# Performance work log

Measured on AMD Instinct MI355X. Metric: run time of the kernel, lower is better.

The kernel has to match this reference:

```python
import jax, jax.numpy as jnp
import numpy as np

DIM = 256
HEADS = 8
WS = 8
N = WS * WS
HID = 1024
EPS = 1e-5


def _rel_pos_index():
    ch, cw = np.meshgrid(np.arange(WS), np.arange(WS), indexing='ij')
    coords = np.stack([ch.ravel(), cw.ravel()])  # [2, N]
    rel = coords[:, :, None] - coords[:, None, :]  # [2, N, N]
    rel = rel.transpose(1, 2, 0).astype(np.int64)
    rel[:, :, 0] += WS - 1
    rel[:, :, 1] += WS - 1
    rel[:, :, 0] *= 2 * WS - 1
    return jnp.asarray(rel.sum(-1))  # [N, N]

REL_IDX = _rel_pos_index()


def layer_norm(x, g, b):
    mu = jnp.mean(x, axis=-1, keepdims=True)
    var = jnp.mean(jnp.square(x - mu), axis=-1, keepdims=True)
    return (x - mu) * jax.lax.rsqrt(var + EPS) * g + b


def setup_inputs() -> dict:
    key = jax.random.key(0)
    ks = jax.random.split(key, 12)
    s = 0.02
    return {
        'x': jax.random.normal(ks[0], (32, 4096, DIM), jnp.float32),
        'attn_mask': jnp.zeros((64, N, N), jnp.float32),  # unused (forward sets mask=None)
        'g1': jnp.ones((DIM,), jnp.float32),
        'b1': jnp.zeros((DIM,), jnp.float32),
        'w_qkv': jax.random.normal(ks[1], (3 * DIM, DIM), jnp.float32) * s,
        'b_qkv': jnp.zeros((3 * DIM,), jnp.float32),
        'bias_table': jax.random.normal(ks[2], ((2 * WS - 1) ** 2, HEADS), jnp.float32) * s,
        'w_proj': jax.random.normal(ks[3], (DIM, DIM), jnp.float32) * s,
        'b_proj': jnp.zeros((DIM,), jnp.float32),
        'g2': jnp.ones((DIM,), jnp.float32),
        'b2': jnp.zeros((DIM,), jnp.float32),
        'w_fc1': jax.random.normal(ks[4], (HID, DIM), jnp.float32) * s,
        'b_fc1': jnp.zeros((HID,), jnp.float32),
        'w_fc2': jax.random.normal(ks[5], (DIM, HID), jnp.float32) * s,
        'b_fc2': jnp.zeros((DIM,), jnp.float32),
    }


def reference(x, attn_mask, g1, b1, w_qkv, b_qkv, bias_table, w_proj, b_proj,
              g2, b2, w_fc1, b_fc1, w_fc2, b_fc2):
    B, L, C = x.shape
    H = W = int(np.sqrt(L))
    hd = C // HEADS
    scale = hd ** -0.5

    shortcut = x
    xn = layer_norm(x, g1, b1).reshape(B, H, W, C)
    xw = xn.reshape(B, H // WS, WS, W // WS, WS, C)
    xw = xw.transpose(0, 1, 3, 2, 4, 5).reshape(-1, N, C)  # [B_, N, C]

    qkv = (xw @ w_qkv.T + b_qkv).reshape(-1, N, 3, HEADS, hd)
    q, k, v = [qkv[:, :, i].transpose(0, 2, 1, 3) for i in range(3)]  # [B_, h, N, d]
    attn = jnp.einsum('bhnd,bhmd->bhnm', q * scale, k)
    bias = bias_table[REL_IDX]  # [N, N, h]
    attn = attn + bias.transpose(2, 0, 1)[None]
    attn = jax.nn.softmax(attn, axis=-1)
    out = jnp.einsum('bhnm,bhmd->bhnd', attn, v)
    out = out.transpose(0, 2, 1, 3).reshape(-1, N, C)
    out = out @ w_proj.T + b_proj

    # window reverse
    out = out.reshape(B, H // WS, W // WS, WS, WS, C)
    out = out.transpose(0, 1, 3, 2, 4, 5).reshape(B, L, C)

    x1 = shortcut + out
    h = layer_norm(x1, g2, b2) @ w_fc1.T + b_fc1
    h = jax.nn.gelu(h, approximate=False)
    return x1 + (h @ w_fc2.T + b_fc2)
```

## Files before the change

### kernel.cpp

```cpp
#include <hip/hip_runtime.h>
#include <hip/hip_bf16.h>
#include <hip/hip_fp16.h>

typedef _Float16 f16;
typedef __attribute__((ext_vector_type(8))) _Float16 f16x8;
typedef __attribute__((ext_vector_type(4))) _Float16 f16x4;
typedef __attribute__((ext_vector_type(2))) _Float16 f16x2;
typedef __attribute__((ext_vector_type(4))) float f32x4;

#define AS1(p) ((const __attribute__((address_space(1))) void*)(p))
#define AS3(p) ((__attribute__((address_space(3))) void*)(p))

__global__ __launch_bounds__(256) void cvt_weights(
    const float* __restrict__ wq, const float* __restrict__ wp,
    const float* __restrict__ wf1, const float* __restrict__ wf2,
    f16* __restrict__ o) {
  int i = blockIdx.x * 256 + threadIdx.x;
  float v;
  if (i < 196608)       v = wq[i];
  else if (i < 262144)  v = wp[i - 196608];
  else if (i < 524288)  v = wf1[i - 262144];
  else                  v = wf2[i - 524288];
  o[i] = (f16)v;
}

__global__ __launch_bounds__(256) void prep_bias(
    const float* __restrict__ bt, float* __restrict__ T) {
  const int flat = blockIdx.x * 256 + threadIdx.x;
  const int h = flat >> 12, l = (flat >> 6) & 63, s = flat & 63;
  const int i = s >> 4, j = (s >> 2) & 3, r = s & 3;
  const int n = 16 * i + 4 * (l >> 4) + r;
  const int m = 16 * j + (l & 15);
  const int idx = ((n >> 3) - (m >> 3) + 7) * 15 + ((n & 7) - (m & 7) + 7);
  T[flat] = bt[idx * 8 + h] * 1.4426950408889634f;
}

template<bool PART, typename TIN>
__global__ __launch_bounds__(256) void ln_rows(
    const TIN* __restrict__ x, const float* __restrict__ g,
    const float* __restrict__ b, f16* __restrict__ out) {
  const int t = blockIdx.x * 4 + (threadIdx.x >> 6);
  const int lane = threadIdx.x & 63;
  float v0, v1, v2, v3;
  if constexpr (sizeof(TIN) == 4) {
    const float4 v = ((const float4*)(x + (long)t * 256))[lane];
    v0 = v.x; v1 = v.y; v2 = v.z; v3 = v.w;
  } else {
    const f16x4 v = ((const f16x4*)(x + (long)t * 256))[lane];
    v0 = (float)v[0]; v1 = (float)v[1]; v2 = (float)v[2]; v3 = (float)v[3];
  }
  float s  = v0 + v1 + v2 + v3;
  float ss = v0*v0 + v1*v1 + v2*v2 + v3*v3;
  #pragma unroll
  for (int off = 32; off; off >>= 1) {
    s  += __shfl_xor(s, off);
    ss += __shfl_xor(ss, off);
  }
  const float mu = s * (1.0f / 256.0f);
  const float var = ss * (1.0f / 256.0f) - mu * mu;
  const float rs = rsqrtf(var + 1e-5f);
  const float4 gv = ((const float4*)g)[lane];
  const float4 bv = ((const float4*)b)[lane];
  long row;
  if (PART) {
    const int bI = t >> 12, l = t & 4095;
    const int hh = l >> 6, w2 = l & 63;
    const int wi = bI * 64 + (hh >> 3) * 8 + (w2 >> 3);
    const int n  = (hh & 7) * 8 + (w2 & 7);
    row = (long)wi * 64 + n;
  } else {
    row = t;
  }
  f16x4 o4;
  o4[0] = (f16)((v0 - mu) * rs * gv.x + bv.x);
  o4[1] = (f16)((v1 - mu) * rs * gv.y + bv.y);
  o4[2] = (f16)((v2 - mu) * rs * gv.z + bv.z);
  o4[3] = (f16)((v3 - mu) * rs * gv.w + bv.w);
  *(f16x4*)(out + row * 256 + lane * 4) = o4;
}

template<int EPI, int K>
__global__ __launch_bounds__(256) void gemm_bt(
    const f16* __restrict__ A, const f16* __restrict__ Bw,
    const float* __restrict__ bias, const float* __restrict__ residf,
    const f16* __restrict__ residh,
    f16* __restrict__ outh, float* __restrict__ outf, int N) {
  __shared__ f16 As[128 * 32];
  __shared__ f16 Bs[128 * 32];
  const int tid  = threadIdx.x;
  const int wid  = tid >> 6;
  const int lane = tid & 63;
  const int qd   = lane >> 4;
  const int l16  = lane & 15;
  const int gx  = gridDim.x;
  const int nwg = gx * gridDim.y;
  const int g   = blockIdx.y * gx + blockIdx.x;
  const int gs  = (g & 7) * (nwg >> 3) + (g >> 3);
  const long tM = (long)(gs / gx) * 128;
  const int  tN = (gs % gx) * 128;
  const int srow = lane >> 2;
  const int scol = (lane & 3) * 8;
  const int wm = (wid >> 1) * 64;
  const int wn = (wid & 1) * 64;

  f32x4 acc[4][4];
  #pragma unroll
  for (int i = 0; i < 4; ++i)
    #pragma unroll
    for (int j = 0; j < 4; ++j) acc[i][j] = (f32x4){0.f, 0.f, 0.f, 0.f};

  for (int k0 = 0; k0 < K; k0 += 32) {
    #pragma unroll
    for (int t = 0; t < 2; ++t) {
      const int gidx = wid * 2 + t;
      const int row  = gidx * 16 + srow;
      __builtin_amdgcn_global_load_lds(AS1(A + (tM + row) * K + k0 + scol),
                                       AS3(&As[gidx * 512]), 16, 0, 0);
      __builtin_amdgcn_global_load_lds(AS1(Bw + (long)(tN + row) * K + k0 + scol),
                                       AS3(&Bs[gidx * 512]), 16, 0, 0);
    }
    __syncthreads();
    f16x8 af[4], bf[4];
    #pragma unroll
    for (int i = 0; i < 4; ++i) af[i] = *(const f16x8*)&As[(wm + i * 16 + l16) * 32 + qd * 8];
    #pragma unroll
    for (int j = 0; j < 4; ++j) bf[j] = *(const f16x8*)&Bs[(wn + j * 16 + l16) * 32 + qd * 8];
    #pragma unroll
    for (int i = 0; i < 4; ++i)
      #pragma unroll
      for (int j = 0; j < 4; ++j)
        acc[i][j] = __builtin_amdgcn_mfma_f32_16x16x32_f16(af[i], bf[j], acc[i][j], 0, 0, 0);
    __syncthreads();
  }

  float bb[4];
  #pragma unroll
  for (int j = 0; j < 4; ++j) bb[j] = bias[tN + wn + j * 16 + l16];

  if (EPI == 3) {
    #pragma unroll
    for (int j = 0; j < 4; ++j) {
      const int col = tN + wn + j * 16 + l16;
      #pragma unroll
      for (int i = 0; i < 4; ++i) {
        #pragma unroll
        for (int r = 0; r < 4; ++r) {
          const long row = tM + wm + i * 16 + qd * 4 + r;
          const long off = row * 256 + col;
          outf[off] = (float)residh[off] + acc[i][j][r] + bb[j];
        }
      }
    }
  } else {
    f16* slice = As + wid * 1024;
    const int rrow = lane >> 3;
    const int seg  = lane & 7;
    #pragma unroll
    for (int i = 0; i < 4; ++i) {
      #pragma unroll
      for (int j = 0; j < 4; ++j) {
        #pragma unroll
        for (int r = 0; r < 4; ++r) {
          float v = acc[i][j][r] + bb[j];
          if (EPI == 2) v = 0.5f * v * (1.0f + erff(v * 0.70710678118654752f));
          const int r16 = qd * 4 + r;
          slice[r16 * 64 + ((j * 16 + l16) ^ ((r16 & 7) << 3))] = (f16)v;
        }
      }
      __syncthreads();
      #pragma unroll
      for (int hrow = 0; hrow < 16; hrow += 8) {
        const int lrow = hrow + rrow;
        const f16x8 v8 = *(const f16x8*)(slice + lrow * 64 + (seg ^ (lrow & 7)) * 8);
        const long grow = tM + wm + i * 16 + lrow;
        const int  gc   = tN + wn + seg * 8;
        if (EPI == 1) {
          const int rw = (int)grow;
          const int wi = rw >> 6, n = rw & 63;
          const int bI = wi >> 6, wloc = wi & 63;
          const int hh = (wloc >> 3) * 8 + (n >> 3);
          const int w2 = (wloc & 7) * 8 + (n & 7);
          const long prow = (long)bI * 4096 + hh * 64 + w2;
          const float* rp = residf + prow * 256 + gc;
          f16x8 o;
          #pragma unroll
          for (int k = 0; k < 8; ++k) o[k] = (f16)(rp[k] + (float)v8[k]);
          *(f16x8*)(outh + prow * 256 + gc) = o;
        } else {
          *(f16x8*)(outh + grow * N + gc) = v8;
        }
      }
      __syncthreads();
    }
  }
}

__global__ __launch_bounds__(256, 3) void attn_win(
    const f16* __restrict__ qkv, const float* __restrict__ bt,
    f16* __restrict__ out) {
  __shared__ __align__(16) char SMEM[4 * 12800];
  const int wid = threadIdx.x >> 6, lane = threadIdx.x & 63;
  const int qd = lane >> 4, l16 = lane & 15;
  const int unit = blockIdx.x * 4 + wid;
  const int wi = unit >> 3, h = unit & 7;
  char* W = SMEM + wid * 12800;
  f16* VT = (f16*)W;
  char* Pb = W + 4608;

  const f16* qbase = qkv + (long)wi * 64 * 768 + h * 32;

  f16x8 qa[4], kb[4];
  #pragma unroll
  for (int i = 0; i < 4; ++i)
    qa[i] = *(const f16x8*)(qbase + (16 * i + l16) * 768 + qd * 8);
  #pragma unroll
  for (int j = 0; j < 4; ++j)
    kb[j] = *(const f16x8*)(qbase + 256 + (16 * j + l16) * 768 + qd * 8);

  #pragma unroll
  for (int it = 0; it < 4; ++it) {
    const f16x8 v8 = *(const f16x8*)(qbase + 512 + (16 * it + l16) * 768 + qd * 8);
    #pragma unroll
    for (int e = 0; e < 8; ++e)
      VT[(qd * 8 + e) * 72 + 16 * it + l16] = v8[e];
  }

  f32x4 S[4][4];
  #pragma unroll
  for (int i = 0; i < 4; ++i)
    #pragma unroll
    for (int j = 0; j < 4; ++j) S[i][j] = (f32x4){0.f, 0.f, 0.f, 0.f};
  #pragma unroll
  for (int i = 0; i < 4; ++i)
    #pragma unroll
    for (int j = 0; j < 4; ++j)
      S[i][j] = __builtin_amdgcn_mfma_f32_16x16x32_f16(qa[i], kb[j], S[i][j], 0, 0, 0);

  const float SC = 0.17677669529663687f * 1.4426950408889634f;
  const float* Tb = bt + ((h * 64 + lane) << 6);
  #pragma unroll
  for (int i = 0; i < 4; ++i) {
    f32x4 b0 = *(const f32x4*)(Tb + i * 16);
    f32x4 b1 = *(const f32x4*)(Tb + i * 16 + 4);
    f32x4 b2 = *(const f32x4*)(Tb + i * 16 + 8);
    f32x4 b3 = *(const f32x4*)(Tb + i * 16 + 12);
    #pragma unroll
    for (int r = 0; r < 4; ++r) {
      S[i][0][r] = S[i][0][r] * SC + b0[r];
      S[i][1][r] = S[i][1][r] * SC + b1[r];
      S[i][2][r] = S[i][2][r] * SC + b2[r];
      S[i][3][r] = S[i][3][r] * SC + b3[r];
    }
  }

  float inv[4][4];
  #pragma unroll
  for (int i = 0; i < 4; ++i) {
    #pragma unroll
    for (int r = 0; r < 4; ++r) {
      float mx = fmaxf(fmaxf(S[i][0][r], S[i][1][r]), fmaxf(S[i][2][r], S[i][3][r]));
      #pragma unroll
      for (int msk = 1; msk < 16; msk <<= 1) mx = fmaxf(mx, __shfl_xor(mx, msk));
      float s0 = 0.f;
      #pragma unroll
      for (int j = 0; j < 4; ++j) {
        const float p = __builtin_amdgcn_exp2f(S[i][j][r] - mx);
        S[i][j][r] = p;
        s0 += p;
      }
      #pragma unroll
      for (int msk = 1; msk < 16; msk <<= 1) s0 += __shfl_xor(s0, msk);
      inv[i][r] = __builtin_amdgcn_rcpf(s0);
    }
  }

  #pragma unroll
  for (int i = 0; i < 4; ++i) {
    #pragma unroll
    for (int r = 0; r < 4; ++r) {
      const int n = 16 * i + 4 * qd + r;
      char* rowp = Pb + n * 128;
      const int sw = (n & 7) << 4;
      #pragma unroll
      for (int j = 0; j < 4; ++j)
        *(f16*)(rowp + ((j * 32 + l16 * 2) ^ sw)) = (f16)S[i][j][r];
    }
  }

  f32x4 O[4][2];
  #pragma unroll
  for (int i = 0; i < 4; ++i) {
    O[i][0] = (f32x4){0.f, 0.f, 0.f, 0.f};
    O[i][1] = (f32x4){0.f, 0.f, 0.f, 0.f};
  }
  #pragma unroll
  for (int kk = 0; kk < 2; ++kk) {
    f16x8 vb[2];
    #pragma unroll
    for (int jj = 0; jj < 2; ++jj)
      vb[jj] = *(const f16x8*)((const char*)W + (16 * jj + l16) * 144 + kk * 64 + qd * 16);
    #pragma unroll
    for (int i = 0; i < 4; ++i) {
      const f16x8 pa = *(const f16x8*)(Pb + (16 * i + l16) * 128 +
                                       ((kk * 64 + qd * 16) ^ ((l16 & 7) << 4)));
      #pragma unroll
      for (int jj = 0; jj < 2; ++jj)
        O[i][jj] = __builtin_amdgcn_mfma_f32_16x16x32_f16(pa, vb[jj], O[i][jj], 0, 0, 0);
    }
  }

  #pragma unroll
  for (int i = 0; i < 4; ++i) {
    #pragma unroll
    for (int jj = 0; jj < 2; ++jj) {
      #pragma unroll
      for (int r = 0; r < 4; ++r) {
        const int n = 16 * i + 4 * qd + r;
        *(f16*)(Pb + n * 80 + jj * 32 + l16 * 2) = (f16)(O[i][jj][r] * inv[i][r]);
      }
    }
  }
  #pragma unroll
  for (int it = 0; it < 4; ++it) {
    const int row = 16 * it + l16;
    const f16x8 o8 = *(const f16x8*)(Pb + row * 80 + qd * 16);
    *(f16x8*)(out + ((long)wi * 64 + row) * 256 + h * 32 + qd * 8) = o8;
  }
}

extern "C" void kernel_launch(void* const* d_in, const int* in_sizes, int n_in,
                              void* d_out, int out_size, void* d_ws, size_t ws_size,
                              hipStream_t stream) {
  const float* x     = (const float*)d_in[0];
  const float* g1    = (const float*)d_in[2];
  const float* b1    = (const float*)d_in[3];
  const float* wqkv  = (const float*)d_in[4];
  const float* bqkv  = (const float*)d_in[5];
  const float* btab  = (const float*)d_in[6];
  const float* wproj = (const float*)d_in[7];
  const float* bproj = (const float*)d_in[8];
  const float* g2    = (const float*)d_in[9];
  const float* b2    = (const float*)d_in[10];
  const float* wfc1  = (const float*)d_in[11];
  const float* bfc1  = (const float*)d_in[12];
  const float* wfc2  = (const float*)d_in[13];
  const float* bfc2  = (const float*)d_in[14];
  float* out = (float*)d_out;

  char* ws = (char*)d_ws;
  f16* wgt   = (f16*)ws;
  f16* wq16  = wgt;
  f16* wp16  = wgt + 196608;
  f16* wf116 = wgt + 262144;
  f16* wf216 = wgt + 524288;
  float* Tbuf = (float*)(ws + 1572864);

  int CH = 1;
  for (int cand = 32; cand >= 1; cand >>= 1) {
    const size_t need = 2097152ULL + (size_t)cand * 12582912ULL;
    if (need <= ws_size) { CH = cand; break; }
  }
  const int NC = 32 / CH;

  const size_t O_xn  = 2097152ULL;
  const size_t O_qkv = O_xn  + (size_t)CH * 2097152ULL;
  const size_t O_x1  = O_qkv + (size_t)CH * 6291456ULL;
  const size_t O_xn2 = O_x1  + (size_t)CH * 2097152ULL;
  f16* xnw  = (f16*)(ws + O_xn);
  f16* qkvb = (f16*)(ws + O_qkv);
  f16* x1h  = (f16*)(ws + O_x1);
  f16* xn2  = (f16*)(ws + O_xn2);
  f16* hbuf = (f16*)(ws + O_xn);

  cvt_weights<<<3072, 256, 0, stream>>>(wqkv, wproj, wfc1, wfc2, wgt);
  prep_bias<<<128, 256, 0, stream>>>(btab, Tbuf);

  const long imgElems = 4096L * 256;
  for (int c = 0; c < NC; ++c) {
    const float* xc  = x   + (long)c * CH * imgElems;
    float*       oc  = out + (long)c * CH * imgElems;
    ln_rows<true, float><<<CH * 1024, 256, 0, stream>>>(xc, g1, b1, xnw);
    gemm_bt<0, 256><<<dim3(6, CH * 32), 256, 0, stream>>>(xnw, wq16, bqkv, nullptr, nullptr, qkvb, nullptr, 768);
    attn_win<<<CH * 128, 256, 0, stream>>>(qkvb, Tbuf, xnw);
    gemm_bt<1, 256><<<dim3(2, CH * 32), 256, 0, stream>>>(xnw, wp16, bproj, xc, nullptr, x1h, nullptr, 256);
    ln_rows<false, f16><<<CH * 1024, 256, 0, stream>>>(x1h, g2, b2, xn2);
    gemm_bt<2, 256><<<dim3(8, CH * 32), 256, 0, stream>>>(xn2, wf116, bfc1, nullptr, nullptr, hbuf, nullptr, 1024);
    gemm_bt<3, 1024><<<dim3(2, CH * 32), 256, 0, stream>>>(hbuf, wf216, bfc2, nullptr, x1h, nullptr, oc, 256);
  }
}
```

Before: 799.9 us.

## Double-buffer GEMM LDS tiles and XOR-swizzle k-chunks to avoid bank conflicts

The GEMM main loop now uses two LDS buffers for A and B. The next k-tile is prefetched with global_load_lds while MFMAs run on the current tile, replacing the load-sync-compute-sync sequence with a single waitcnt and barrier per iteration. The k-chunk column used when loading into LDS and when reading fragments out of it is XOR-swizzled by row, to reduce LDS bank conflicts on the f16x8 fragment reads. The cost is double the LDS footprint, which may lower occupancy, and a correctness dependence on the store swizzle and read swizzle matching.

Result: no change. 801.7 us (+0.2%).

```diff
diff --git a/kernel.cpp b/kernel.cpp
--- a/kernel.cpp
+++ b/kernel.cpp
@@ -85,8 +85,8 @@
     const float* __restrict__ bias, const float* __restrict__ residf,
     const f16* __restrict__ residh,
     f16* __restrict__ outh, float* __restrict__ outf, int N) {
-  __shared__ f16 As[128 * 32];
-  __shared__ f16 Bs[128 * 32];
+  __shared__ f16 As[2][128 * 32];
+  __shared__ f16 Bs[2][128 * 32];
   const int tid  = threadIdx.x;
   const int wid  = tid >> 6;
   const int lane = tid & 63;
@@ -99,9 +99,10 @@
   const long tM = (long)(gs / gx) * 128;
   const int  tN = (gs % gx) * 128;
   const int srow = lane >> 2;
-  const int scol = (lane & 3) * 8;
+  const int scol = ((lane & 3) ^ ((srow >> 1) & 3)) * 8;
   const int wm = (wid >> 1) * 64;
   const int wn = (wid & 1) * 64;
+  const int rsw = (l16 >> 1) & 3;
 
   f32x4 acc[4][4];
   #pragma unroll
@@ -109,28 +110,49 @@
     #pragma unroll
     for (int j = 0; j < 4; ++j) acc[i][j] = (f32x4){0.f, 0.f, 0.f, 0.f};
 
-  for (int k0 = 0; k0 < K; k0 += 32) {
-    #pragma unroll
-    for (int t = 0; t < 2; ++t) {
-      const int gidx = wid * 2 + t;
-      const int row  = gidx * 16 + srow;
-      __builtin_amdgcn_global_load_lds(AS1(A + (tM + row) * K + k0 + scol),
-                                       AS3(&As[gidx * 512]), 16, 0, 0);
-      __builtin_amdgcn_global_load_lds(AS1(Bw + (long)(tN + row) * K + k0 + scol),
-                                       AS3(&Bs[gidx * 512]), 16, 0, 0);
-    }
-    __syncthreads();
+  const int nt = K / 32;
+
+  #pragma unroll
+  for (int t = 0; t < 2; ++t) {
+    const int gidx = wid * 2 + t;
+    const int row  = gidx * 16 + srow;
+    __builtin_amdgcn_global_load_lds(AS1(A + (tM + row) * K + scol),
+                                     AS3(&As[0][gidx * 512]), 16, 0, 0);
+    __builtin_amdgcn_global_load_lds(AS1(Bw + (long)(tN + row) * K + scol),
+                                     AS3(&Bs[0][gidx * 512]), 16, 0, 0);
+  }
+  asm volatile("s_waitcnt vmcnt(0)" ::: "memory");
+  __builtin_amdgcn_s_barrier();
+
+  int cur = 0;
+  for (int t = 0; t < nt; ++t) {
+    if (t + 1 < nt) {
+      const int k0 = (t + 1) * 32;
+      #pragma unroll
+      for (int u = 0; u < 2; ++u) {
+        const int gidx = wid * 2 + u;
+        const int row  = gidx * 16 + srow;
+        __builtin_amdgcn_global_load_lds(AS1(A + (tM + row) * K + k0 + scol),
+                                         AS3(&As[cur ^ 1][gidx * 512]), 16, 0, 0);
+        __builtin_amdgcn_global_load_lds(AS1(Bw + (long)(tN + row) * K + k0 + scol),
+                                         AS3(&Bs[cur ^ 1][gidx * 512]), 16, 0, 0);
+      }
+    }
     f16x8 af[4], bf[4];
     #pragma unroll
-    for (int i = 0; i < 4; ++i) af[i] = *(const f16x8*)&As[(wm + i * 16 + l16) * 32 + qd * 8];
-    #pragma unroll
-    for (int j = 0; j < 4; ++j) bf[j] = *(const f16x8*)&Bs[(wn + j * 16 + l16) * 32 + qd * 8];
+    for (int i = 0; i < 4; ++i)
+      af[i] = *(const f16x8*)&As[cur][(wm + i * 16 + l16) * 32 + ((qd ^ rsw) * 8)];
+    #pragma unroll
+    for (int j = 0; j < 4; ++j)
+      bf[j] = *(const f16x8*)&Bs[cur][(wn + j * 16 + l16) * 32 + ((qd ^ rsw) * 8)];
     #pragma unroll
     for (int i = 0; i < 4; ++i)
       #pragma unroll
       for (int j = 0; j < 4; ++j)
         acc[i][j] = __builtin_amdgcn_mfma_f32_16x16x32_f16(af[i], bf[j], acc[i][j], 0, 0, 0);
-    __syncthreads();
+    asm volatile("s_waitcnt vmcnt(0)" ::: "memory");
+    __builtin_amdgcn_s_barrier();
+    cur ^= 1;
   }
 
   float bb[4];
@@ -152,7 +174,7 @@
       }
     }
   } else {
-    f16* slice = As + wid * 1024;
+    f16* slice = &As[0][0] + wid * 1024;
     const int rrow = lane >> 3;
     const int seg  = lane & 7;
     #pragma unroll
```
